# Kernel tuning notes

Hardware: AMD Instinct MI355X
Metric: run time of the kernel (lower is better)

Reference implementation:

```python
import jax, jax.numpy as jnp
import numpy as np

TEMPERATURE = 0.5

def setup_inputs() -> dict:
    key = jax.random.key(0)
    k1, k2 = jax.random.split(key)
    emb_i = jax.random.normal(k1, (4096, 128), dtype=jnp.float32)
    emb_j = jax.random.normal(k2, (4096, 128), dtype=jnp.float32)
    return {"emb_i": emb_i, "emb_j": emb_j}

def reference(emb_i, emb_j):
    B = emb_i.shape[0]
    eps = 1e-12
    z_i = emb_i / jnp.maximum(jnp.linalg.norm(emb_i, axis=1, keepdims=True), eps)
    z_j = emb_j / jnp.maximum(jnp.linalg.norm(emb_j, axis=1, keepdims=True), eps)
    z = jnp.concatenate([z_i, z_j], axis=0)  # [2B, D]
    # cosine similarity of normalized vectors == dot product (GEMM instead of O(N^2 D) broadcast)
    sim = z @ z.T  # [2B, 2B]
    sim_ij = jnp.einsum('bd,bd->b', z_i, z_j)  # diag(sim, +B)
    positives = jnp.concatenate([sim_ij, sim_ij], axis=0)  # diag(sim,-B) == diag(sim,+B)
    neg_mask = 1.0 - jnp.eye(2 * B, dtype=sim.dtype)
    denom = jnp.sum(neg_mask * jnp.exp(sim / TEMPERATURE), axis=1)  # [2B]
    loss_partial = -(positives / TEMPERATURE - jnp.log(denom))
    return jnp.sum(loss_partial) / (2 * B)
```

## Files before the change

kernel.cpp:

```cpp
#include <hip/hip_runtime.h>
#include <hip/hip_bf16.h>
#include <math.h>

#define BB       4096
#define N2       8192
#define DIMS     128
#define NT       64
#define NJOBS    (NT * (NT + 1) / 2)
#define TILE     128
#define LDS_PAD  8
#define LDS_ROWW (DIMS + LDS_PAD)

#define ZSCALE   1.6986436f
#define DIAG_E2  7.38905609893065f

typedef __attribute__((ext_vector_type(8))) short short8;
typedef __attribute__((ext_vector_type(4))) float float4v;

__global__ __launch_bounds__(256) void norm_kernel(
    const float* __restrict__ emb_i, const float* __restrict__ emb_j,
    __hip_bfloat16* __restrict__ z, float* __restrict__ pos,
    float* __restrict__ out) {
  if (blockIdx.x == 0 && threadIdx.x == 0) out[0] = 0.0f;

  int gw   = (blockIdx.x * blockDim.x + threadIdx.x) >> 6;
  int lane = threadIdx.x & 63;
  if (gw >= BB) return;

  const float2* ei = (const float2*)(emb_i + (size_t)gw * DIMS);
  const float2* ej = (const float2*)(emb_j + (size_t)gw * DIMS);
  float2 a = ei[lane];
  float2 b = ej[lane];

  float sa = a.x * a.x + a.y * a.y;
  float sb = b.x * b.x + b.y * b.y;
  #pragma unroll
  for (int m = 32; m; m >>= 1) {
    sa += __shfl_xor(sa, m, 64);
    sb += __shfl_xor(sb, m, 64);
  }
  float inva = 1.0f / fmaxf(sqrtf(sa), 1e-12f);
  float invb = 1.0f / fmaxf(sqrtf(sb), 1e-12f);

  float zi0 = a.x * inva, zi1 = a.y * inva;
  float zj0 = b.x * invb, zj1 = b.y * invb;

  float p = zi0 * zj0 + zi1 * zj1;
  #pragma unroll
  for (int m = 32; m; m >>= 1) p += __shfl_xor(p, m, 64);
  if (lane == 0) pos[gw] = p;

  __hip_bfloat162* zr_i = (__hip_bfloat162*)(z + (size_t)gw * DIMS);
  __hip_bfloat162* zr_j = (__hip_bfloat162*)(z + (size_t)(gw + BB) * DIMS);
  __hip_bfloat162 vi, vj;
  vi.x = __float2bfloat16(zi0 * ZSCALE); vi.y = __float2bfloat16(zi1 * ZSCALE);
  vj.x = __float2bfloat16(zj0 * ZSCALE); vj.y = __float2bfloat16(zj1 * ZSCALE);
  zr_i[lane] = vi;
  zr_j[lane] = vj;
}

__global__ __launch_bounds__(256, 4) void simloss_sym(
    const __hip_bfloat16* __restrict__ z, float* __restrict__ P) {
  __shared__ short lds[TILE * LDS_ROWW];
  __shared__ float csum_lds[4][TILE];

  const int tid  = threadIdx.x;
  const int wave = tid >> 6;
  const int lane = tid & 63;
  const int lr   = lane & 15;
  const int quad = lane >> 4;

  const int j = blockIdx.x;
  int I = (int)((129.0f - sqrtf(16641.0f - 8.0f * (float)j)) * 0.5f);
  I = I < 0 ? 0 : (I > NT - 1 ? NT - 1 : I);
  while (I < NT - 1 && (I + 1) * (2 * NT - I) / 2 <= j) ++I;
  while (I > 0 && I * (2 * NT - I + 1) / 2 > j) --I;
  const int J = I + (j - I * (2 * NT - I + 1) / 2);
  const bool diag = (I == J);
  const int R0 = I * TILE;
  const int C0 = J * TILE;

  const ushort* zp = (const ushort*)z;

  short8 afrag[2][4];
  #pragma unroll
  for (int rt = 0; rt < 2; rt++) {
    const int arow = R0 + wave * 32 + rt * 16 + lr;
    const short8* ap = (const short8*)(zp + (size_t)arow * DIMS + quad * 8);
    afrag[rt][0] = ap[0];
    afrag[rt][1] = ap[4];
    afrag[rt][2] = ap[8];
    afrag[rt][3] = ap[12];
  }

  {
    const short8* src = (const short8*)(zp + (size_t)C0 * DIMS);
    #pragma unroll
    for (int i = 0; i < 8; i++) {
      int idx  = tid + 256 * i;
      int row  = idx >> 4;
      int col8 = idx & 15;
      *(short8*)&lds[row * LDS_ROWW + col8 * 8] = src[idx];
    }
  }
  __syncthreads();

  float rowsum[2][4];
  #pragma unroll
  for (int rt = 0; rt < 2; rt++)
    #pragma unroll
    for (int r = 0; r < 4; r++) rowsum[rt][r] = 0.0f;

  #pragma unroll 2
  for (int t = 0; t < 8; t++) {
    const short8* bp = (const short8*)&lds[(t * 16 + lr) * LDS_ROWW + quad * 8];
    short8 b0 = bp[0];
    short8 b1 = bp[4];
    short8 b2 = bp[8];
    short8 b3 = bp[12];
    float ctile = 0.0f;
    #pragma unroll
    for (int rt = 0; rt < 2; rt++) {
      float4v acc = {0.0f, 0.0f, 0.0f, 0.0f};
      acc = __builtin_amdgcn_mfma_f32_16x16x32_bf16(afrag[rt][0], b0, acc, 0, 0, 0);
      acc = __builtin_amdgcn_mfma_f32_16x16x32_bf16(afrag[rt][1], b1, acc, 0, 0, 0);
      acc = __builtin_amdgcn_mfma_f32_16x16x32_bf16(afrag[rt][2], b2, acc, 0, 0, 0);
      acc = __builtin_amdgcn_mfma_f32_16x16x32_bf16(afrag[rt][3], b3, acc, 0, 0, 0);
      #pragma unroll
      for (int r = 0; r < 4; r++) {
        float e = __builtin_amdgcn_exp2f(acc[r]);
        rowsum[rt][r] += e;
        ctile += e;
      }
    }
    if (!diag) {
      ctile += __shfl_xor(ctile, 16, 64);
      ctile += __shfl_xor(ctile, 32, 64);
      if (quad == 0) csum_lds[wave][t * 16 + lr] = ctile;
    }
  }

  #pragma unroll
  for (int m = 1; m < 16; m <<= 1)
    #pragma unroll
    for (int rt = 0; rt < 2; rt++)
      #pragma unroll
      for (int r = 0; r < 4; r++)
        rowsum[rt][r] += __shfl_xor(rowsum[rt][r], m, 64);
  if (lr == 0) {
    float* Prow = P + ((size_t)I * NT + J) * TILE + wave * 32;
    #pragma unroll
    for (int rt = 0; rt < 2; rt++) {
      float4v v = {rowsum[rt][0], rowsum[rt][1], rowsum[rt][2], rowsum[rt][3]};
      *(float4v*)&Prow[rt * 16 + quad * 4] = v;
    }
  }

  if (!diag) {
    __syncthreads();
    if (tid < TILE) {
      float s = csum_lds[0][tid] + csum_lds[1][tid] +
                csum_lds[2][tid] + csum_lds[3][tid];
      P[((size_t)J * NT + I) * TILE + tid] = s;
    }
  }
}

__global__ __launch_bounds__(128) void reduce_rows(
    const float* __restrict__ P, const float* __restrict__ pos,
    float* __restrict__ out) {
  __shared__ double sred[128];
  const int tid = threadIdx.x;
  const int r   = blockIdx.x * 128 + tid;
  const int I   = r >> 7;
  const int rr  = r & (TILE - 1);

  const float* p = P + (size_t)I * NT * TILE + rr;
  float acc = 0.0f;
  #pragma unroll 8
  for (int J = 0; J < NT; J++) acc += p[(size_t)J * TILE];

  double term = (double)(logf(acc - DIAG_E2) - 2.0f * pos[r & (BB - 1)]) /
                (double)N2;
  sred[tid] = term;
  __syncthreads();
  #pragma unroll
  for (int s = 64; s; s >>= 1) {
    if (tid < s) sred[tid] += sred[tid + s];
    __syncthreads();
  }
  if (tid == 0) atomicAdd(out, (float)sred[0]);
}

extern "C" void kernel_launch(void* const* d_in, const int* in_sizes, int n_in,
                              void* d_out, int out_size, void* d_ws, size_t ws_size,
                              hipStream_t stream) {
  const float* emb_i = (const float*)d_in[0];
  const float* emb_j = (const float*)d_in[1];

  __hip_bfloat16* z = (__hip_bfloat16*)d_ws;
  float* pos   = (float*)((char*)d_ws + (size_t)N2 * DIMS * 2);
  float* P     = pos + BB;

  norm_kernel<<<BB / 4, 256, 0, stream>>>(emb_i, emb_j, z, pos, (float*)d_out);
  simloss_sym<<<NJOBS, 256, 0, stream>>>(z, P);
  reduce_rows<<<N2 / 128, 128, 0, stream>>>(P, pos, (float*)d_out);
}
```

Before: 82.28 us.

## Fuse row normalization into similarity kernel and recompute positives in reduction

Drops the separate normalization kernel. Each similarity tile block now reads fp32 embeddings directly, computes row norms, and packs scaled bf16 fragments for both the A registers and the LDS B tile. The reduction kernel recomputes the positive-pair dot products from the raw inputs and uses a wave-level shuffle reduction in place of a shared-memory tree. This saves one launch and the bf16 z round trip through memory. In exchange, every tile reads twice as many bytes as fp32 and redoes the normalization work for each of the 2080 jobs, and the zeroing of out inside block 0 is unordered relative to other blocks.

```diff
diff --git a/kernel.cpp b/kernel.cpp
--- a/kernel.cpp
+++ b/kernel.cpp
@@ -17,50 +17,22 @@
 typedef __attribute__((ext_vector_type(8))) short short8;
 typedef __attribute__((ext_vector_type(4))) float float4v;
 
-__global__ __launch_bounds__(256) void norm_kernel(
+static __device__ __forceinline__ short bfb(float x) {
+  __hip_bfloat16 h = __float2bfloat16(x);
+  return *reinterpret_cast<short*>(&h);
+}
+static __device__ __forceinline__ short8 pack8(float4 a, float4 b, float inv) {
+  short8 o;
+  o[0] = bfb(a.x * inv); o[1] = bfb(a.y * inv);
+  o[2] = bfb(a.z * inv); o[3] = bfb(a.w * inv);
+  o[4] = bfb(b.x * inv); o[5] = bfb(b.y * inv);
+  o[6] = bfb(b.z * inv); o[7] = bfb(b.w * inv);
+  return o;
+}
+
+__global__ __launch_bounds__(256, 4) void simloss_fused(
     const float* __restrict__ emb_i, const float* __restrict__ emb_j,
-    __hip_bfloat16* __restrict__ z, float* __restrict__ pos,
-    float* __restrict__ out) {
-  if (blockIdx.x == 0 && threadIdx.x == 0) out[0] = 0.0f;
-
-  int gw   = (blockIdx.x * blockDim.x + threadIdx.x) >> 6;
-  int lane = threadIdx.x & 63;
-  if (gw >= BB) return;
-
-  const float2* ei = (const float2*)(emb_i + (size_t)gw * DIMS);
-  const float2* ej = (const float2*)(emb_j + (size_t)gw * DIMS);
-  float2 a = ei[lane];
-  float2 b = ej[lane];
-
-  float sa = a.x * a.x + a.y * a.y;
-  float sb = b.x * b.x + b.y * b.y;
-  #pragma unroll
-  for (int m = 32; m; m >>= 1) {
-    sa += __shfl_xor(sa, m, 64);
-    sb += __shfl_xor(sb, m, 64);
-  }
-  float inva = 1.0f / fmaxf(sqrtf(sa), 1e-12f);
-  float invb = 1.0f / fmaxf(sqrtf(sb), 1e-12f);
-
-  float zi0 = a.x * inva, zi1 = a.y * inva;
-  float zj0 = b.x * invb, zj1 = b.y * invb;
-
-  float p = zi0 * zj0 + zi1 * zj1;
-  #pragma unroll
-  for (int m = 32; m; m >>= 1) p += __shfl_xor(p, m, 64);
-  if (lane == 0) pos[gw] = p;
-
-  __hip_bfloat162* zr_i = (__hip_bfloat162*)(z + (size_t)gw * DIMS);
-  __hip_bfloat162* zr_j = (__hip_bfloat162*)(z + (size_t)(gw + BB) * DIMS);
-  __hip_bfloat162 vi, vj;
-  vi.x = __float2bfloat16(zi0 * ZSCALE); vi.y = __float2bfloat16(zi1 * ZSCALE);
-  vj.x = __float2bfloat16(zj0 * ZSCALE); vj.y = __float2bfloat16(zj1 * ZSCALE);
-  zr_i[lane] = vi;
-  zr_j[lane] = vj;
-}
-
-__global__ __launch_bounds__(256, 4) void simloss_sym(
-    const __hip_bfloat16* __restrict__ z, float* __restrict__ P) {
+    float* __restrict__ P, float* __restrict__ out) {
   __shared__ short lds[TILE * LDS_ROWW];
   __shared__ float csum_lds[4][TILE];
 
@@ -69,6 +41,8 @@
   const int lane = tid & 63;
   const int lr   = lane & 15;
   const int quad = lane >> 4;
+
+  if (blockIdx.x == 0 && tid == 0) out[0] = 0.0f;
 
   const int j = blockIdx.x;
   int I = (int)((129.0f - sqrtf(16641.0f - 8.0f * (float)j)) * 0.5f);
@@ -80,28 +54,52 @@
   const int R0 = I * TILE;
   const int C0 = J * TILE;
 
-  const ushort* zp = (const ushort*)z;
-
   short8 afrag[2][4];
   #pragma unroll
   for (int rt = 0; rt < 2; rt++) {
-    const int arow = R0 + wave * 32 + rt * 16 + lr;
-    const short8* ap = (const short8*)(zp + (size_t)arow * DIMS + quad * 8);
-    afrag[rt][0] = ap[0];
-    afrag[rt][1] = ap[4];
-    afrag[rt][2] = ap[8];
-    afrag[rt][3] = ap[12];
+    const int g = R0 + wave * 32 + rt * 16 + lr;
+    const float4* bp4 = (const float4*)(g < BB
+        ? emb_i + (size_t)g * DIMS
+        : emb_j + (size_t)(g - BB) * DIMS);
+    float4 v[8];
+    float s = 0.0f;
+    #pragma unroll
+    for (int k = 0; k < 4; k++) {
+      float4 a = bp4[quad * 2 + 8 * k];
+      float4 b = bp4[quad * 2 + 8 * k + 1];
+      v[2 * k] = a; v[2 * k + 1] = b;
+      s += a.x * a.x + a.y * a.y + a.z * a.z + a.w * a.w;
+      s += b.x * b.x + b.y * b.y + b.z * b.z + b.w * b.w;
+    }
+    s += __shfl_xor(s, 16, 64);
+    s += __shfl_xor(s, 32, 64);
+    const float inv = ZSCALE / fmaxf(sqrtf(s), 1e-12f);
+    #pragma unroll
+    for (int k = 0; k < 4; k++)
+      afrag[rt][k] = pack8(v[2 * k], v[2 * k + 1], inv);
   }
 
   {
-    const short8* src = (const short8*)(zp + (size_t)C0 * DIMS);
-    #pragma unroll
-    for (int i = 0; i < 8; i++) {
-      int idx  = tid + 256 * i;
-      int row  = idx >> 4;
-      int col8 = idx & 15;
-      *(short8*)&lds[row * LDS_ROWW + col8 * 8] = src[idx];
-    }
+    const int row  = tid >> 1;
+    const int half = tid & 1;
+    const int g    = C0 + row;
+    const float4* src = (const float4*)(g < BB
+        ? emb_i + (size_t)g * DIMS
+        : emb_j + (size_t)(g - BB) * DIMS) + half * 16;
+    float4 v[16];
+    float s = 0.0f;
+    #pragma unroll
+    for (int k = 0; k < 16; k++) {
+      float4 a = src[k];
+      v[k] = a;
+      s += a.x * a.x + a.y * a.y + a.z * a.z + a.w * a.w;
+    }
+    s += __shfl_xor(s, 1, 64);
+    const float inv = ZSCALE / fmaxf(sqrtf(s), 1e-12f);
+    short* dst = &lds[row * LDS_ROWW + half * 64];
+    #pragma unroll
+    for (int w = 0; w < 8; w++)
+      *(short8*)&dst[w * 8] = pack8(v[2 * w], v[2 * w + 1], inv);
   }
   __syncthreads();
 
@@ -166,12 +164,11 @@
   }
 }
 
-__global__ __launch_bounds__(128) void reduce_rows(
-    const float* __restrict__ P, const float* __restrict__ pos,
-    float* __restrict__ out) {
-  __shared__ double sred[128];
+__global__ __launch_bounds__(64) void reduce_pos(
+    const float* __restrict__ P, const float* __restrict__ emb_i,
+    const float* __restrict__ emb_j, float* __restrict__ out) {
   const int tid = threadIdx.x;
-  const int r   = blockIdx.x * 128 + tid;
+  const int r   = blockIdx.x * 64 + tid;
   const int I   = r >> 7;
   const int rr  = r & (TILE - 1);
 
@@ -180,16 +177,25 @@
   #pragma unroll 8
   for (int J = 0; J < NT; J++) acc += p[(size_t)J * TILE];
 
-  double term = (double)(logf(acc - DIAG_E2) - 2.0f * pos[r & (BB - 1)]) /
-                (double)N2;
-  sred[tid] = term;
-  __syncthreads();
-  #pragma unroll
-  for (int s = 64; s; s >>= 1) {
-    if (tid < s) sred[tid] += sred[tid + s];
-    __syncthreads();
-  }
-  if (tid == 0) atomicAdd(out, (float)sred[0]);
+  const int g = r & (BB - 1);
+  const float4* xi = (const float4*)(emb_i + (size_t)g * DIMS);
+  const float4* xj = (const float4*)(emb_j + (size_t)g * DIMS);
+  float si = 0.0f, sj = 0.0f, sij = 0.0f;
+  #pragma unroll
+  for (int k = 0; k < 32; k++) {
+    float4 a = xi[k], b = xj[k];
+    si  += a.x * a.x + a.y * a.y + a.z * a.z + a.w * a.w;
+    sj  += b.x * b.x + b.y * b.y + b.z * b.z + b.w * b.w;
+    sij += a.x * b.x + a.y * b.y + a.z * b.z + a.w * b.w;
+  }
+  const float invi = 1.0f / fmaxf(sqrtf(si), 1e-12f);
+  const float invj = 1.0f / fmaxf(sqrtf(sj), 1e-12f);
+  const float pos  = sij * invi * invj;
+
+  double term = (double)(logf(acc - DIAG_E2) - 2.0f * pos) / (double)N2;
+  #pragma unroll
+  for (int m = 32; m; m >>= 1) term += __shfl_xor(term, m, 64);
+  if (tid == 0) atomicAdd(out, (float)term);
 }
 
 extern "C" void kernel_launch(void* const* d_in, const int* in_sizes, int n_in,
@@ -198,11 +204,8 @@
   const float* emb_i = (const float*)d_in[0];
   const float* emb_j = (const float*)d_in[1];
 
-  __hip_bfloat16* z = (__hip_bfloat16*)d_ws;
-  float* pos   = (float*)((char*)d_ws + (size_t)N2 * DIMS * 2);
-  float* P     = pos + BB;
-
-  norm_kernel<<<BB / 4, 256, 0, stream>>>(emb_i, emb_j, z, pos, (float*)d_out);
-  simloss_sym<<<NJOBS, 256, 0, stream>>>(z, P);
-  reduce_rows<<<N2 / 128, 128, 0, stream>>>(P, pos, (float*)d_out);
-}
+  float* P = (float*)d_ws;
+
+  simloss_fused<<<NJOBS, 256, 0, stream>>>(emb_i, emb_j, P, (float*)d_out);
+  reduce_pos<<<N2 / 64, 64, 0, stream>>>(P, emb_i, emb_j, (float*)d_out);
+}
```

After: 100.2 us. 1.22x slower.

## Drop LDS staging in simloss; write per-wave column sums to global

Applied to the files above, without the earlier changes.

The B tile is no longer staged into shared memory; each wave loads its B fragments straight from global (L2-cached) memory. This removes both __syncthreads and the LDS footprint, which may raise occupancy. Per-wave column partial sums now go to a new global buffer Pc, and reduce_rows folds the four wave partials for lower-triangle tiles. The cost is redundant global loads of B across the four waves and extra partial-sum traffic. The unroll of the tile loop also goes from 2 to 4.

```diff
diff --git a/kernel.cpp b/kernel.cpp
--- a/kernel.cpp
+++ b/kernel.cpp
@@ -8,8 +8,6 @@
 #define NT       64
 #define NJOBS    (NT * (NT + 1) / 2)
 #define TILE     128
-#define LDS_PAD  8
-#define LDS_ROWW (DIMS + LDS_PAD)
 
 #define ZSCALE   1.6986436f
 #define DIAG_E2  7.38905609893065f
@@ -60,10 +58,8 @@
 }
 
 __global__ __launch_bounds__(256, 4) void simloss_sym(
-    const __hip_bfloat16* __restrict__ z, float* __restrict__ P) {
-  __shared__ short lds[TILE * LDS_ROWW];
-  __shared__ float csum_lds[4][TILE];
-
+    const __hip_bfloat16* __restrict__ z, float* __restrict__ P,
+    float* __restrict__ Pc) {
   const int tid  = threadIdx.x;
   const int wave = tid >> 6;
   const int lane = tid & 63;
@@ -93,27 +89,16 @@
     afrag[rt][3] = ap[12];
   }
 
-  {
-    const short8* src = (const short8*)(zp + (size_t)C0 * DIMS);
-    #pragma unroll
-    for (int i = 0; i < 8; i++) {
-      int idx  = tid + 256 * i;
-      int row  = idx >> 4;
-      int col8 = idx & 15;
-      *(short8*)&lds[row * LDS_ROWW + col8 * 8] = src[idx];
-    }
-  }
-  __syncthreads();
-
   float rowsum[2][4];
   #pragma unroll
   for (int rt = 0; rt < 2; rt++)
     #pragma unroll
     for (int r = 0; r < 4; r++) rowsum[rt][r] = 0.0f;
 
-  #pragma unroll 2
+  #pragma unroll 4
   for (int t = 0; t < 8; t++) {
-    const short8* bp = (const short8*)&lds[(t * 16 + lr) * LDS_ROWW + quad * 8];
+    const short8* bp =
+        (const short8*)(zp + (size_t)(C0 + t * 16 + lr) * DIMS + quad * 8);
     short8 b0 = bp[0];
     short8 b1 = bp[4];
     short8 b2 = bp[8];
@@ -136,7 +121,8 @@
     if (!diag) {
       ctile += __shfl_xor(ctile, 16, 64);
       ctile += __shfl_xor(ctile, 32, 64);
-      if (quad == 0) csum_lds[wave][t * 16 + lr] = ctile;
+      if (quad == 0)
+        Pc[(((size_t)J * NT + I) * 4 + wave) * TILE + t * 16 + lr] = ctile;
     }
   }
 
@@ -155,30 +141,26 @@
       *(float4v*)&Prow[rt * 16 + quad * 4] = v;
     }
   }
-
-  if (!diag) {
-    __syncthreads();
-    if (tid < TILE) {
-      float s = csum_lds[0][tid] + csum_lds[1][tid] +
-                csum_lds[2][tid] + csum_lds[3][tid];
-      P[((size_t)J * NT + I) * TILE + tid] = s;
-    }
-  }
 }
 
 __global__ __launch_bounds__(128) void reduce_rows(
-    const float* __restrict__ P, const float* __restrict__ pos,
-    float* __restrict__ out) {
+    const float* __restrict__ P, const float* __restrict__ Pc,
+    const float* __restrict__ pos, float* __restrict__ out) {
   __shared__ double sred[128];
   const int tid = threadIdx.x;
   const int r   = blockIdx.x * 128 + tid;
-  const int I   = r >> 7;
+  const int X   = r >> 7;
   const int rr  = r & (TILE - 1);
 
-  const float* p = P + (size_t)I * NT * TILE + rr;
   float acc = 0.0f;
-  #pragma unroll 8
-  for (int J = 0; J < NT; J++) acc += p[(size_t)J * TILE];
+  for (int Y = 0; Y < NT; Y++) {
+    if (Y >= X) {
+      acc += P[((size_t)X * NT + Y) * TILE + rr];
+    } else {
+      const float* pc = Pc + ((size_t)X * NT + Y) * 4 * TILE + rr;
+      acc += pc[0] + pc[TILE] + pc[2 * TILE] + pc[3 * TILE];
+    }
+  }
 
   double term = (double)(logf(acc - DIAG_E2) - 2.0f * pos[r & (BB - 1)]) /
                 (double)N2;
@@ -199,10 +181,11 @@
   const float* emb_j = (const float*)d_in[1];
 
   __hip_bfloat16* z = (__hip_bfloat16*)d_ws;
-  float* pos   = (float*)((char*)d_ws + (size_t)N2 * DIMS * 2);
-  float* P     = pos + BB;
+  float* pos = (float*)((char*)d_ws + (size_t)N2 * DIMS * 2);
+  float* P   = pos + BB;
+  float* Pc  = P + (size_t)NT * NT * TILE;
 
   norm_kernel<<<BB / 4, 256, 0, stream>>>(emb_i, emb_j, z, pos, (float*)d_out);
-  simloss_sym<<<NJOBS, 256, 0, stream>>>(z, P);
-  reduce_rows<<<N2 / 128, 128, 0, stream>>>(P, pos, (float*)d_out);
+  simloss_sym<<<NJOBS, 256, 0, stream>>>(z, P, Pc);
+  reduce_rows<<<NT, 128, 0, stream>>>(P, Pc, pos, (float*)d_out);
 }
```

Measured after the change: 120.4 us. +46.3%, slower.
